# Kernel optimization log

Measured on AMD Instinct MI355X. Metric: run time of the kernel, lower is better.

Reference implementation:

```python
import jax, jax.numpy as jnp
import numpy as np

N_NODES = 50000
N_EDGES = 800000
IN_C, HID_C, OUT_C = 128, 96, 64
BN_EPS = 1e-5


def setup_inputs() -> dict:
    key = jax.random.key(0)
    ks = jax.random.split(key, 12)
    x = jax.random.normal(ks[0], (N_NODES, IN_C), dtype=jnp.float32)
    edge_weight = jax.random.uniform(ks[1], (N_EDGES,), dtype=jnp.float32)
    row = jax.random.randint(ks[2], (N_EDGES,), 0, N_NODES, dtype=jnp.int32)
    col = jax.random.randint(ks[3], (N_EDGES,), 0, N_NODES, dtype=jnp.int32)
    s = 0.05
    W1 = jax.random.normal(ks[4], (IN_C, HID_C), dtype=jnp.float32) * s
    b1 = jnp.zeros((HID_C,), dtype=jnp.float32)
    W2 = jax.random.normal(ks[5], (HID_C, HID_C), dtype=jnp.float32) * s
    b2 = jnp.zeros((HID_C,), dtype=jnp.float32)
    W3 = jax.random.normal(ks[6], (HID_C, OUT_C), dtype=jnp.float32) * s
    b3 = jnp.zeros((OUT_C,), dtype=jnp.float32)
    g1 = jnp.ones((HID_C,), dtype=jnp.float32)
    be1 = jnp.zeros((HID_C,), dtype=jnp.float32)
    g2 = jnp.ones((HID_C,), dtype=jnp.float32)
    be2 = jnp.zeros((HID_C,), dtype=jnp.float32)
    return {"x": x, "edge_weight": edge_weight, "row": row, "col": col,
            "W1": W1, "b1": b1, "W2": W2, "b2": b2, "W3": W3, "b3": b3,
            "g1": g1, "be1": be1, "g2": g2, "be2": be2}


def _gcn_conv(h, edge_weight, row, col, W, b):
    # GCNConv: adj_norm @ (h @ W) + b, adj in COO with normalized edge_weight
    h = h @ W  # [N, d_out]
    msg = edge_weight[:, None] * h[col]  # gather + scale: [E, d_out]
    agg = jax.ops.segment_sum(msg, row, num_segments=N_NODES)  # scatter-add
    return agg + b


def _batch_norm(h, gamma, beta):
    # BatchNorm1d (training-mode batch statistics, biased variance)
    mean = jnp.mean(h, axis=0)
    var = jnp.var(h, axis=0)
    return (h - mean) * jax.lax.rsqrt(var + BN_EPS) * gamma + beta


def reference(x, edge_weight, row, col, W1, b1, W2, b2, W3, b3, g1, be1, g2, be2):
    h = _gcn_conv(x, edge_weight, row, col, W1, b1)
    h = jax.nn.relu(_batch_norm(h, g1, be1))  # dropout is identity in eval
    h = _gcn_conv(h, edge_weight, row, col, W2, b2)
    h = jax.nn.relu(_batch_norm(h, g2, be2))
    h = _gcn_conv(h, edge_weight, row, col, W3, b3)
    return jax.nn.log_softmax(h, axis=-1)
```

## Files before the change

kernel.cpp:

```cpp
#include <hip/hip_runtime.h>
#include <hip/hip_bf16.h>
#include <math.h>

#define N_NODES 50000
#define N_EDGES 800000
#define IN_C 128
#define HID_C 96
#define OUT_C 64
#define BN_EPS 1e-5f

#define ELL_SHIFT 6
#define ELL_CAP   64

#define NGRP 8
#define GRP_ROWS ((N_NODES + NGRP - 1) / NGRP)

#define EW_SCALE 65535.0f
#define EW_INV   (1.0f / 65535.0f)

#define ST_SLICES 4

typedef __attribute__((ext_vector_type(8))) short short8;
typedef __attribute__((ext_vector_type(4))) float f32x4;

static __device__ __forceinline__ unsigned short f2b(float f) {
    __hip_bfloat16 b = __float2bfloat16(f);
    return *reinterpret_cast<unsigned short*>(&b);
}
static __device__ __forceinline__ float b2f(unsigned short u) {
    return __uint_as_float((unsigned)u << 16);
}
static __device__ __forceinline__ unsigned pack2(float a, float b) {
    return (unsigned)f2b(a) | ((unsigned)f2b(b) << 16);
}

#define FMA8(B, V, W)                                          \
    acc[(B) + 0] += (W) * __uint_as_float((V).x << 16);        \
    acc[(B) + 1] += (W) * __uint_as_float((V).x & 0xffff0000u);\
    acc[(B) + 2] += (W) * __uint_as_float((V).y << 16);        \
    acc[(B) + 3] += (W) * __uint_as_float((V).y & 0xffff0000u);\
    acc[(B) + 4] += (W) * __uint_as_float((V).z << 16);        \
    acc[(B) + 5] += (W) * __uint_as_float((V).z & 0xffff0000u);\
    acc[(B) + 6] += (W) * __uint_as_float((V).w << 16);        \
    acc[(B) + 7] += (W) * __uint_as_float((V).w & 0xffff0000u);

__global__ void prep_all(const float* __restrict__ W1, const float* __restrict__ W2,
                         const float* __restrict__ W3,
                         unsigned short* __restrict__ Wt1,
                         unsigned short* __restrict__ Wt2,
                         unsigned short* __restrict__ Wt3,
                         int* __restrict__ cnt, float* __restrict__ stats) {
    int i = blockIdx.x * blockDim.x + threadIdx.x;
    const int n1 = IN_C * HID_C, n2 = HID_C * HID_C, n3 = HID_C * OUT_C;
    if (i < n1) {
        int j = i / IN_C, k = i % IN_C;
        Wt1[i] = f2b(W1[k * HID_C + j]);
    } else if (i < n1 + n2) {
        int t = i - n1, j = t / HID_C, k = t % HID_C;
        Wt2[t] = f2b(W2[k * HID_C + j]);
    } else if (i < n1 + n2 + n3) {
        int t = i - n1 - n2, j = t / HID_C, k = t % HID_C;
        Wt3[t] = f2b(W3[k * OUT_C + j]);
    }
    if (i < N_NODES) cnt[i] = 0;
    if (i < 2 * ST_SLICES * 2 * HID_C) stats[i] = 0.f;
}

__global__ __launch_bounds__(256)
void fill_ell(const int* __restrict__ row, const int* __restrict__ col,
              const float* __restrict__ ew, int* __restrict__ cnt,
              unsigned int* __restrict__ pairs) {
    int g = blockIdx.x & (NGRP - 1);
    int e = (blockIdx.x >> 3) * 256 + threadIdx.x;
    if (e >= N_EDGES) return;
    int r = row[e];
    int lo = g * GRP_ROWS;
    if ((unsigned)(r - lo) >= (unsigned)GRP_ROWS) return;
    int slot = atomicAdd(&cnt[r], 1);
    if (slot < ELL_CAP) {
        unsigned wq = (unsigned)(ew[e] * EW_SCALE + 0.5f);
        pairs[((size_t)r << ELL_SHIFT) + slot] =
            (wq << 16) | (unsigned)col[e];
    }
}

template <int K, int J, bool APPLY, bool XBF16>
__global__ __launch_bounds__(256)
void gemm_mfma(const void* __restrict__ xin,
               const unsigned short* __restrict__ Wt,
               const float* __restrict__ stats,
               const float* __restrict__ gamma,
               const float* __restrict__ beta,
               unsigned short* __restrict__ h, int N) {
    constexpr int MT = 64;
    constexpr int SK = K + 8;
    constexpr int NT = J / 16;
    __shared__ unsigned short Xs[MT * SK];
    __shared__ unsigned short Ws[J * SK];
    __shared__ float scsh_s[APPLY ? 2 * K : 2];

    int tid = threadIdx.x;
    int tileBase = blockIdx.x * MT;

    if (APPLY) {
        if (tid < K) {
            float s = 0.f, sq = 0.f;
#pragma unroll
            for (int sl = 0; sl < ST_SLICES; ++sl) {
                s  += stats[sl * 2 * K + tid];
                sq += stats[sl * 2 * K + K + tid];
            }
            const float invN = 1.f / N_NODES;
            float mean = s * invN;
            float var = sq * invN - mean * mean;
            float sc = gamma[tid] * rsqrtf(var + BN_EPS);
            scsh_s[tid] = sc;
            scsh_s[K + tid] = beta[tid] - mean * sc;
        }
        __syncthreads();
    }

    if (XBF16) {
        const unsigned short* xb = (const unsigned short*)xin;
        for (int i = tid; i < MT * (K / 8); i += 256) {
            int node = i / (K / 8), kq = i % (K / 8);
            int gn = min(tileBase + node, N - 1);
            const unsigned short* src = xb + (size_t)gn * K + kq * 8;
            ushort4 u0 = *(const ushort4*)(src);
            ushort4 u1 = *(const ushort4*)(src + 4);
            if (APPLY) {
                int kb = kq * 8;
                float v0 = fmaxf(b2f(u0.x) * scsh_s[kb + 0] + scsh_s[K + kb + 0], 0.f);
                float v1 = fmaxf(b2f(u0.y) * scsh_s[kb + 1] + scsh_s[K + kb + 1], 0.f);
                float v2 = fmaxf(b2f(u0.z) * scsh_s[kb + 2] + scsh_s[K + kb + 2], 0.f);
                float v3 = fmaxf(b2f(u0.w) * scsh_s[kb + 3] + scsh_s[K + kb + 3], 0.f);
                float v4 = fmaxf(b2f(u1.x) * scsh_s[kb + 4] + scsh_s[K + kb + 4], 0.f);
                float v5 = fmaxf(b2f(u1.y) * scsh_s[kb + 5] + scsh_s[K + kb + 5], 0.f);
                float v6 = fmaxf(b2f(u1.z) * scsh_s[kb + 6] + scsh_s[K + kb + 6], 0.f);
                float v7 = fmaxf(b2f(u1.w) * scsh_s[kb + 7] + scsh_s[K + kb + 7], 0.f);
                u0 = make_ushort4(f2b(v0), f2b(v1), f2b(v2), f2b(v3));
                u1 = make_ushort4(f2b(v4), f2b(v5), f2b(v6), f2b(v7));
            }
            *(ushort4*)&Xs[node * SK + kq * 8] = u0;
            *(ushort4*)&Xs[node * SK + kq * 8 + 4] = u1;
        }
    } else {
        const float* xf = (const float*)xin;
        for (int i = tid; i < MT * (K / 4); i += 256) {
            int node = i / (K / 4), kq = i % (K / 4);
            int gn = min(tileBase + node, N - 1);
            float4 v = *(const float4*)(xf + (size_t)gn * K + kq * 4);
            ushort4 o = make_ushort4(f2b(v.x), f2b(v.y), f2b(v.z), f2b(v.w));
            *(ushort4*)&Xs[node * SK + kq * 4] = o;
        }
    }
    for (int i = tid; i < J * (K / 4); i += 256) {
        int j = i / (K / 4), kq = i % (K / 4);
        *(ushort4*)&Ws[j * SK + kq * 4] =
            *(const ushort4*)(Wt + (size_t)j * K + kq * 4);
    }
    __syncthreads();

    int lane = tid & 63;
    int w = tid >> 6;
    int m16 = lane & 15;
    int quad = lane >> 4;

    f32x4 acc[NT];
#pragma unroll
    for (int nt = 0; nt < NT; ++nt) acc[nt] = (f32x4){0.f, 0.f, 0.f, 0.f};

    const unsigned short* xrow = &Xs[(w * 16 + m16) * SK];
#pragma unroll
    for (int k0 = 0; k0 < K; k0 += 32) {
        short8 a = *(const short8*)(xrow + k0 + quad * 8);
#pragma unroll
        for (int nt = 0; nt < NT; ++nt) {
            short8 b = *(const short8*)&Ws[(nt * 16 + m16) * SK + k0 + quad * 8];
            acc[nt] = __builtin_amdgcn_mfma_f32_16x16x32_bf16(a, b, acc[nt], 0, 0, 0);
        }
    }

#pragma unroll
    for (int nt = 0; nt < NT; ++nt) {
#pragma unroll
        for (int r = 0; r < 4; ++r) {
            int node = tileBase + w * 16 + quad * 4 + r;
            if (node < N)
                h[(size_t)node * J + nt * 16 + m16] = f2b(acc[nt][r]);
        }
    }
}

template <int D, bool LSM, bool STATS>
__global__ __launch_bounds__(256)
void agg_fused(const unsigned short* __restrict__ h,
               const int* __restrict__ cnt,
               const unsigned int* __restrict__ pairs,
               unsigned short* __restrict__ outb,
               float* __restrict__ outf,
               const float* __restrict__ b3,
               float* __restrict__ stats) {
    constexpr int TPN = 4;
    constexpr int C = D / TPN;
    constexpr int NPB = 256 / TPN;
    __shared__ float shS[STATS ? 16 * C : 1];
    __shared__ float shQ[STATS ? 16 * C : 1];

    int tid = threadIdx.x;
    int q = tid & 3;
    int nloc = tid >> 2;
    int n = blockIdx.x * NPB + nloc;
    bool valid = n < N_NODES;
    int nn = valid ? n : N_NODES - 1;
    int end = valid ? min(cnt[nn], ELL_CAP) : 0;
    const unsigned* ep = pairs + ((size_t)nn << ELL_SHIFT);
    const int cbase = q * C;

    float acc[C];
#pragma unroll
    for (int c = 0; c < C; ++c) acc[c] = 0.f;

    int i = 0;
    for (; i + 1 < end; i += 2) {
        unsigned p0 = ep[i], p1 = ep[i + 1];
        float w0 = (float)(p0 >> 16) * EW_INV;
        float w1 = (float)(p1 >> 16) * EW_INV;
        const unsigned short* r0 = h + (size_t)(p0 & 0xFFFFu) * D + cbase;
        const unsigned short* r1 = h + (size_t)(p1 & 0xFFFFu) * D + cbase;
        uint4 v0[C / 8], v1[C / 8];
#pragma unroll
        for (int ch = 0; ch < C / 8; ++ch) v0[ch] = *(const uint4*)(r0 + ch * 8);
#pragma unroll
        for (int ch = 0; ch < C / 8; ++ch) v1[ch] = *(const uint4*)(r1 + ch * 8);
#pragma unroll
        for (int ch = 0; ch < C / 8; ++ch) { FMA8(ch * 8, v0[ch], w0) }
#pragma unroll
        for (int ch = 0; ch < C / 8; ++ch) { FMA8(ch * 8, v1[ch], w1) }
    }
    if (i < end) {
        unsigned p0 = ep[i];
        float w0 = (float)(p0 >> 16) * EW_INV;
        const unsigned short* r0 = h + (size_t)(p0 & 0xFFFFu) * D + cbase;
#pragma unroll
        for (int ch = 0; ch < C / 8; ++ch) {
            uint4 v = *(const uint4*)(r0 + ch * 8);
            FMA8(ch * 8, v, w0)
        }
    }

    if (LSM) {
        float v[C];
#pragma unroll
        for (int c = 0; c < C; ++c) v[c] = acc[c] + b3[cbase + c];
        float m = v[0];
#pragma unroll
        for (int c = 1; c < C; ++c) m = fmaxf(m, v[c]);
        m = fmaxf(m, __shfl_xor(m, 1));
        m = fmaxf(m, __shfl_xor(m, 2));
        float s = 0.f;
#pragma unroll
        for (int c = 0; c < C; ++c) s += expf(v[c] - m);
        s += __shfl_xor(s, 1);
        s += __shfl_xor(s, 2);
        float l = m + logf(s);
        if (valid) {
#pragma unroll
            for (int ch = 0; ch < C / 4; ++ch) {
                float4 o = make_float4(v[ch * 4 + 0] - l, v[ch * 4 + 1] - l,
                                       v[ch * 4 + 2] - l, v[ch * 4 + 3] - l);
                *(float4*)(outf + (size_t)n * D + cbase + ch * 4) = o;
            }
        }
    } else {
#pragma unroll
        for (int c = 0; c < C; ++c) acc[c] = b2f(f2b(acc[c]));
#pragma unroll
        for (int ch = 0; ch < C / 8; ++ch) {
            uint4 o;
            o.x = pack2(acc[ch * 8 + 0], acc[ch * 8 + 1]);
            o.y = pack2(acc[ch * 8 + 2], acc[ch * 8 + 3]);
            o.z = pack2(acc[ch * 8 + 4], acc[ch * 8 + 5]);
            o.w = pack2(acc[ch * 8 + 6], acc[ch * 8 + 7]);
            if (valid)
                *(uint4*)(outb + (size_t)n * D + cbase + ch * 8) = o;
        }
        if (STATS) {
            int lane = tid & 63;
            int wv = tid >> 6;
#pragma unroll
            for (int c = 0; c < C; ++c) {
                float s = acc[c];
                float sq = s * s;
#pragma unroll
                for (int msk = 4; msk < 64; msk <<= 1) {
                    s  += __shfl_xor(s, msk);
                    sq += __shfl_xor(sq, msk);
                }
                if (lane < 4) {
                    shS[(wv * 4 + lane) * C + c] = s;
                    shQ[(wv * 4 + lane) * C + c] = sq;
                }
            }
            __syncthreads();
            if (tid < D) {
                int qq = tid / C, cl = tid % C;
                float S = 0.f, Q = 0.f;
#pragma unroll
                for (int w2 = 0; w2 < 4; ++w2) {
                    S += shS[(w2 * 4 + qq) * C + cl];
                    Q += shQ[(w2 * 4 + qq) * C + cl];
                }
                int slice = blockIdx.x & (ST_SLICES - 1);
                atomicAdd(&stats[slice * 2 * D + tid], S);
                atomicAdd(&stats[slice * 2 * D + D + tid], Q);
            }
        }
    }
}

extern "C" void kernel_launch(void* const* d_in, const int* in_sizes, int n_in,
                              void* d_out, int out_size, void* d_ws, size_t ws_size,
                              hipStream_t stream) {
    const float* x   = (const float*)d_in[0];
    const float* ew  = (const float*)d_in[1];
    const int*   row = (const int*)d_in[2];
    const int*   col = (const int*)d_in[3];
    const float* W1  = (const float*)d_in[4];
    const float* W2  = (const float*)d_in[6];
    const float* W3  = (const float*)d_in[8];
    const float* b3  = (const float*)d_in[9];
    const float* g1  = (const float*)d_in[10];
    const float* be1 = (const float*)d_in[11];
    const float* g2  = (const float*)d_in[12];
    const float* be2 = (const float*)d_in[13];
    float* out = (float*)d_out;

    unsigned short* B      = (unsigned short*)d_ws;
    unsigned short* A      = B + (size_t)N_NODES * HID_C;
    unsigned short* Wt1    = A + (size_t)N_NODES * HID_C;
    unsigned short* Wt2    = Wt1 + IN_C * HID_C;
    unsigned short* Wt3    = Wt2 + HID_C * HID_C;
    unsigned int*   pairs  = (unsigned int*)(Wt3 + HID_C * OUT_C);
    int*            cnt    = (int*)(pairs + ((size_t)N_NODES << ELL_SHIFT));
    float*          stats1 = (float*)(cnt + N_NODES);
    float*          stats2 = stats1 + ST_SLICES * 2 * HID_C;

    const int T = 256;
    const int gridE  = (N_EDGES + T - 1) / T;
    const int gridG  = (N_NODES + 63) / 64;
    const int gridP  = (N_NODES + T - 1) / T;

    prep_all<<<gridP, T, 0, stream>>>(W1, W2, W3, Wt1, Wt2, Wt3, cnt, stats1);
    fill_ell<<<gridE * NGRP, T, 0, stream>>>(row, col, ew, cnt, pairs);

    gemm_mfma<IN_C, HID_C, false, false><<<gridG, T, 0, stream>>>(
        x, Wt1, nullptr, nullptr, nullptr, A, N_NODES);
    agg_fused<HID_C, false, true><<<gridG, T, 0, stream>>>(
        A, cnt, pairs, B, nullptr, nullptr, stats1);

    gemm_mfma<HID_C, HID_C, true, true><<<gridG, T, 0, stream>>>(
        B, Wt2, stats1, g1, be1, A, N_NODES);
    agg_fused<HID_C, false, true><<<gridG, T, 0, stream>>>(
        A, cnt, pairs, B, nullptr, nullptr, stats2);

    gemm_mfma<HID_C, OUT_C, true, true><<<gridG, T, 0, stream>>>(
        B, Wt3, stats2, g2, be2, A, N_NODES);
    agg_fused<OUT_C, true, false><<<gridG, T, 0, stream>>>(
        A, cnt, pairs, nullptr, out, b3, nullptr);
}
```

Before: 266.2 us.

## Fuse all GCN stages into one cooperative persistent kernel with grid syncs

Replaces the eight separate kernel launches with a single cooperative persistent kernel that loops over tiles and uses grid-wide syncs between phases, and overlaps the ELL fill with the first GEMM. The aim is to remove launch overhead and inter-kernel gaps. The cost is lower parallelism: the grid is capped at 768 blocks with strided tile loops, and the kernel now pays for grid barriers and higher register and LDS use. The old multi-kernel path stays as a fallback if the cooperative launch fails.

```diff
diff --git a/kernel.cpp b/kernel.cpp
--- a/kernel.cpp
+++ b/kernel.cpp
@@ -1,6 +1,9 @@
 #include <hip/hip_runtime.h>
+#include <hip/hip_cooperative_groups.h>
 #include <hip/hip_bf16.h>
 #include <math.h>
+
+namespace cg = cooperative_groups;
 
 #define N_NODES 50000
 #define N_EDGES 800000
@@ -19,6 +22,8 @@
 #define EW_INV   (1.0f / 65535.0f)
 
 #define ST_SLICES 4
+
+#define SMEM_BYTES 43584
 
 typedef __attribute__((ext_vector_type(8))) short short8;
 typedef __attribute__((ext_vector_type(4))) float f32x4;
@@ -44,13 +49,11 @@
     acc[(B) + 6] += (W) * __uint_as_float((V).w << 16);        \
     acc[(B) + 7] += (W) * __uint_as_float((V).w & 0xffff0000u);
 
-__global__ void prep_all(const float* __restrict__ W1, const float* __restrict__ W2,
-                         const float* __restrict__ W3,
-                         unsigned short* __restrict__ Wt1,
-                         unsigned short* __restrict__ Wt2,
-                         unsigned short* __restrict__ Wt3,
-                         int* __restrict__ cnt, float* __restrict__ stats) {
-    int i = blockIdx.x * blockDim.x + threadIdx.x;
+
+static __device__ __forceinline__ void prep_body(
+    int i, const float* W1, const float* W2, const float* W3,
+    unsigned short* Wt1, unsigned short* Wt2, unsigned short* Wt3,
+    int* cnt, float* stats) {
     const int n1 = IN_C * HID_C, n2 = HID_C * HID_C, n3 = HID_C * OUT_C;
     if (i < n1) {
         int j = i / IN_C, k = i % IN_C;
@@ -66,22 +69,327 @@
     if (i < 2 * ST_SLICES * 2 * HID_C) stats[i] = 0.f;
 }
 
+static __device__ __forceinline__ void fill_body(
+    int grp, int e, const int* row, const int* col, const float* ew,
+    int* cnt, unsigned int* pairs) {
+    if (e >= N_EDGES) return;
+    int r = row[e];
+    int lo = grp * GRP_ROWS;
+    if ((unsigned)(r - lo) >= (unsigned)GRP_ROWS) return;
+    int slot = atomicAdd(&cnt[r], 1);
+    if (slot < ELL_CAP) {
+        unsigned wq = (unsigned)(ew[e] * EW_SCALE + 0.5f);
+        pairs[((size_t)r << ELL_SHIFT) + slot] = (wq << 16) | (unsigned)col[e];
+    }
+}
+
+template <int K, int J, bool APPLY, bool XBF16>
+static __device__ __forceinline__ void gemm_phase(
+    unsigned char* smem, const void* xin, const unsigned short* Wt,
+    const float* stats, const float* gamma, const float* beta,
+    unsigned short* h, int gridSz) {
+    constexpr int MT = 64;
+    constexpr int SK = K + 8;
+    constexpr int NT = J / 16;
+    unsigned short* Xs = (unsigned short*)smem;
+    unsigned short* Ws = Xs + MT * SK;
+    float* scsh = (float*)(smem + (size_t)(MT + J) * SK * 2);
+
+    int tid = threadIdx.x;
+
+    if (APPLY) {
+        if (tid < K) {
+            float s = 0.f, sq = 0.f;
+#pragma unroll
+            for (int sl = 0; sl < ST_SLICES; ++sl) {
+                s  += stats[sl * 2 * K + tid];
+                sq += stats[sl * 2 * K + K + tid];
+            }
+            const float invN = 1.f / N_NODES;
+            float mean = s * invN;
+            float var = sq * invN - mean * mean;
+            float sc = gamma[tid] * rsqrtf(var + BN_EPS);
+            scsh[tid] = sc;
+            scsh[K + tid] = beta[tid] - mean * sc;
+        }
+    }
+    for (int i = tid; i < J * (K / 4); i += 256) {
+        int j = i / (K / 4), kq = i % (K / 4);
+        *(ushort4*)&Ws[j * SK + kq * 4] =
+            *(const ushort4*)(Wt + (size_t)j * K + kq * 4);
+    }
+    __syncthreads();
+
+    int lane = tid & 63;
+    int w = tid >> 6;
+    int m16 = lane & 15;
+    int quad = lane >> 4;
+    const int nTiles = (N_NODES + MT - 1) / MT;
+
+    for (int tile = blockIdx.x; tile < nTiles; tile += gridSz) {
+        int tileBase = tile * MT;
+
+        if (XBF16) {
+            const unsigned short* xb = (const unsigned short*)xin;
+            for (int i = tid; i < MT * (K / 8); i += 256) {
+                int node = i / (K / 8), kq = i % (K / 8);
+                int gn = min(tileBase + node, N_NODES - 1);
+                const unsigned short* src = xb + (size_t)gn * K + kq * 8;
+                ushort4 u0 = *(const ushort4*)(src);
+                ushort4 u1 = *(const ushort4*)(src + 4);
+                if (APPLY) {
+                    int kb = kq * 8;
+                    float v0 = fmaxf(b2f(u0.x) * scsh[kb + 0] + scsh[K + kb + 0], 0.f);
+                    float v1 = fmaxf(b2f(u0.y) * scsh[kb + 1] + scsh[K + kb + 1], 0.f);
+                    float v2 = fmaxf(b2f(u0.z) * scsh[kb + 2] + scsh[K + kb + 2], 0.f);
+                    float v3 = fmaxf(b2f(u0.w) * scsh[kb + 3] + scsh[K + kb + 3], 0.f);
+                    float v4 = fmaxf(b2f(u1.x) * scsh[kb + 4] + scsh[K + kb + 4], 0.f);
+                    float v5 = fmaxf(b2f(u1.y) * scsh[kb + 5] + scsh[K + kb + 5], 0.f);
+                    float v6 = fmaxf(b2f(u1.z) * scsh[kb + 6] + scsh[K + kb + 6], 0.f);
+                    float v7 = fmaxf(b2f(u1.w) * scsh[kb + 7] + scsh[K + kb + 7], 0.f);
+                    u0 = make_ushort4(f2b(v0), f2b(v1), f2b(v2), f2b(v3));
+                    u1 = make_ushort4(f2b(v4), f2b(v5), f2b(v6), f2b(v7));
+                }
+                *(ushort4*)&Xs[node * SK + kq * 8] = u0;
+                *(ushort4*)&Xs[node * SK + kq * 8 + 4] = u1;
+            }
+        } else {
+            const float* xf = (const float*)xin;
+            for (int i = tid; i < MT * (K / 4); i += 256) {
+                int node = i / (K / 4), kq = i % (K / 4);
+                int gn = min(tileBase + node, N_NODES - 1);
+                float4 v = *(const float4*)(xf + (size_t)gn * K + kq * 4);
+                ushort4 o = make_ushort4(f2b(v.x), f2b(v.y), f2b(v.z), f2b(v.w));
+                *(ushort4*)&Xs[node * SK + kq * 4] = o;
+            }
+        }
+        __syncthreads();
+
+        f32x4 acc[NT];
+#pragma unroll
+        for (int nt = 0; nt < NT; ++nt) acc[nt] = (f32x4){0.f, 0.f, 0.f, 0.f};
+
+        const unsigned short* xrow = &Xs[(w * 16 + m16) * SK];
+#pragma unroll
+        for (int k0 = 0; k0 < K; k0 += 32) {
+            short8 a = *(const short8*)(xrow + k0 + quad * 8);
+#pragma unroll
+            for (int nt = 0; nt < NT; ++nt) {
+                short8 b = *(const short8*)&Ws[(nt * 16 + m16) * SK + k0 + quad * 8];
+                acc[nt] = __builtin_amdgcn_mfma_f32_16x16x32_bf16(a, b, acc[nt], 0, 0, 0);
+            }
+        }
+
+#pragma unroll
+        for (int nt = 0; nt < NT; ++nt) {
+#pragma unroll
+            for (int r = 0; r < 4; ++r) {
+                int node = tileBase + w * 16 + quad * 4 + r;
+                if (node < N_NODES)
+                    h[(size_t)node * J + nt * 16 + m16] = f2b(acc[nt][r]);
+            }
+        }
+        __syncthreads();
+    }
+}
+
+template <int D, bool LSM, bool STATS>
+static __device__ __forceinline__ void agg_phase(
+    unsigned char* smem, const unsigned short* h, const int* cnt,
+    const unsigned int* pairs, unsigned short* outb, float* outf,
+    const float* b3, float* stats, int gridSz) {
+    constexpr int TPN = 4;
+    constexpr int C = D / TPN;
+    constexpr int NPB = 256 / TPN;
+    float* shS = (float*)smem;
+    float* shQ = shS + 16 * C;
+
+    int tid = threadIdx.x;
+    int q = tid & 3;
+    int nloc = tid >> 2;
+    const int nTiles = (N_NODES + NPB - 1) / NPB;
+
+    for (int tile = blockIdx.x; tile < nTiles; tile += gridSz) {
+        int n = tile * NPB + nloc;
+        bool valid = n < N_NODES;
+        int nn = valid ? n : N_NODES - 1;
+        int end = valid ? min(cnt[nn], ELL_CAP) : 0;
+        const unsigned* ep = pairs + ((size_t)nn << ELL_SHIFT);
+        const int cbase = q * C;
+
+        float acc[C];
+#pragma unroll
+        for (int c = 0; c < C; ++c) acc[c] = 0.f;
+
+        int i = 0;
+        for (; i + 1 < end; i += 2) {
+            unsigned p0 = ep[i], p1 = ep[i + 1];
+            float w0 = (float)(p0 >> 16) * EW_INV;
+            float w1 = (float)(p1 >> 16) * EW_INV;
+            const unsigned short* r0 = h + (size_t)(p0 & 0xFFFFu) * D + cbase;
+            const unsigned short* r1 = h + (size_t)(p1 & 0xFFFFu) * D + cbase;
+            uint4 v0[C / 8], v1[C / 8];
+#pragma unroll
+            for (int ch = 0; ch < C / 8; ++ch) v0[ch] = *(const uint4*)(r0 + ch * 8);
+#pragma unroll
+            for (int ch = 0; ch < C / 8; ++ch) v1[ch] = *(const uint4*)(r1 + ch * 8);
+#pragma unroll
+            for (int ch = 0; ch < C / 8; ++ch) { FMA8(ch * 8, v0[ch], w0) }
+#pragma unroll
+            for (int ch = 0; ch < C / 8; ++ch) { FMA8(ch * 8, v1[ch], w1) }
+        }
+        if (i < end) {
+            unsigned p0 = ep[i];
+            float w0 = (float)(p0 >> 16) * EW_INV;
+            const unsigned short* r0 = h + (size_t)(p0 & 0xFFFFu) * D + cbase;
+#pragma unroll
+            for (int ch = 0; ch < C / 8; ++ch) {
+                uint4 v = *(const uint4*)(r0 + ch * 8);
+                FMA8(ch * 8, v, w0)
+            }
+        }
+
+        if (LSM) {
+            float v[C];
+#pragma unroll
+            for (int c = 0; c < C; ++c) v[c] = acc[c] + b3[cbase + c];
+            float m = v[0];
+#pragma unroll
+            for (int c = 1; c < C; ++c) m = fmaxf(m, v[c]);
+            m = fmaxf(m, __shfl_xor(m, 1));
+            m = fmaxf(m, __shfl_xor(m, 2));
+            float s = 0.f;
+#pragma unroll
+            for (int c = 0; c < C; ++c) s += expf(v[c] - m);
+            s += __shfl_xor(s, 1);
+            s += __shfl_xor(s, 2);
+            float l = m + logf(s);
+            if (valid) {
+#pragma unroll
+                for (int ch = 0; ch < C / 4; ++ch) {
+                    float4 o = make_float4(v[ch * 4 + 0] - l, v[ch * 4 + 1] - l,
+                                           v[ch * 4 + 2] - l, v[ch * 4 + 3] - l);
+                    *(float4*)(outf + (size_t)n * D + cbase + ch * 4) = o;
+                }
+            }
+        } else {
+#pragma unroll
+            for (int c = 0; c < C; ++c) acc[c] = b2f(f2b(acc[c]));
+#pragma unroll
+            for (int ch = 0; ch < C / 8; ++ch) {
+                uint4 o;
+                o.x = pack2(acc[ch * 8 + 0], acc[ch * 8 + 1]);
+                o.y = pack2(acc[ch * 8 + 2], acc[ch * 8 + 3]);
+                o.z = pack2(acc[ch * 8 + 4], acc[ch * 8 + 5]);
+                o.w = pack2(acc[ch * 8 + 6], acc[ch * 8 + 7]);
+                if (valid)
+                    *(uint4*)(outb + (size_t)n * D + cbase + ch * 8) = o;
+            }
+            if (STATS) {
+                int lane = tid & 63;
+                int wv = tid >> 6;
+#pragma unroll
+                for (int c = 0; c < C; ++c) {
+                    float s = acc[c];
+                    float sq = s * s;
+#pragma unroll
+                    for (int msk = 4; msk < 64; msk <<= 1) {
+                        s  += __shfl_xor(s, msk);
+                        sq += __shfl_xor(sq, msk);
+                    }
+                    if (lane < 4) {
+                        shS[(wv * 4 + lane) * C + c] = s;
+                        shQ[(wv * 4 + lane) * C + c] = sq;
+                    }
+                }
+                __syncthreads();
+                if (tid < D) {
+                    int qq = tid / C, cl = tid % C;
+                    float S = 0.f, Q = 0.f;
+#pragma unroll
+                    for (int w2 = 0; w2 < 4; ++w2) {
+                        S += shS[(w2 * 4 + qq) * C + cl];
+                        Q += shQ[(w2 * 4 + qq) * C + cl];
+                    }
+                    int slice = blockIdx.x & (ST_SLICES - 1);
+                    atomicAdd(&stats[slice * 2 * D + tid], S);
+                    atomicAdd(&stats[slice * 2 * D + D + tid], Q);
+                }
+                __syncthreads();
+            }
+        }
+    }
+}
+
+struct MegaParams {
+    const float *x, *ew;
+    const int *row, *col;
+    const float *W1, *W2, *W3, *b3, *g1, *be1, *g2, *be2;
+    unsigned short *B, *A, *Wt1, *Wt2, *Wt3;
+    unsigned int *pairs;
+    int *cnt;
+    float *stats1, *stats2, *out;
+};
+
+__global__ __launch_bounds__(256)
+void mega(MegaParams p) {
+    __shared__ __align__(16) unsigned char smem[SMEM_BYTES];
+    cg::grid_group grid = cg::this_grid();
+    const int G = (int)gridDim.x;
+
+    for (int i = blockIdx.x * 256 + threadIdx.x; i < N_NODES; i += G * 256)
+        prep_body(i, p.W1, p.W2, p.W3, p.Wt1, p.Wt2, p.Wt3, p.cnt, p.stats1);
+    grid.sync();
+
+    gemm_phase<IN_C, HID_C, false, false>(smem, p.x, p.Wt1,
+                                          nullptr, nullptr, nullptr, p.A, G);
+    {
+        const int nUnits = (N_EDGES + 255) / 256;
+        int grp = blockIdx.x & (NGRP - 1);
+        for (int u = blockIdx.x >> 3; u < nUnits; u += (G >> 3))
+            fill_body(grp, u * 256 + threadIdx.x, p.row, p.col, p.ew,
+                      p.cnt, p.pairs);
+    }
+    grid.sync();
+
+    agg_phase<HID_C, false, true>(smem, p.A, p.cnt, p.pairs, p.B,
+                                  nullptr, nullptr, p.stats1, G);
+    grid.sync();
+
+    gemm_phase<HID_C, HID_C, true, true>(smem, p.B, p.Wt2,
+                                         p.stats1, p.g1, p.be1, p.A, G);
+    grid.sync();
+
+    agg_phase<HID_C, false, true>(smem, p.A, p.cnt, p.pairs, p.B,
+                                  nullptr, nullptr, p.stats2, G);
+    grid.sync();
+
+    gemm_phase<HID_C, OUT_C, true, true>(smem, p.B, p.Wt3,
+                                         p.stats2, p.g2, p.be2, p.A, G);
+    grid.sync();
+
+    agg_phase<OUT_C, true, false>(smem, p.A, p.cnt, p.pairs, nullptr,
+                                  p.out, p.b3, nullptr, G);
+}
+
+__global__ void prep_all(const float* __restrict__ W1, const float* __restrict__ W2,
+                         const float* __restrict__ W3,
+                         unsigned short* __restrict__ Wt1,
+                         unsigned short* __restrict__ Wt2,
+                         unsigned short* __restrict__ Wt3,
+                         int* __restrict__ cnt, float* __restrict__ stats) {
+    int i = blockIdx.x * blockDim.x + threadIdx.x;
+    if (i < N_NODES)
+        prep_body(i, W1, W2, W3, Wt1, Wt2, Wt3, cnt, stats);
+}
+
 __global__ __launch_bounds__(256)
 void fill_ell(const int* __restrict__ row, const int* __restrict__ col,
               const float* __restrict__ ew, int* __restrict__ cnt,
               unsigned int* __restrict__ pairs) {
-    int g = blockIdx.x & (NGRP - 1);
+    int grp = blockIdx.x & (NGRP - 1);
     int e = (blockIdx.x >> 3) * 256 + threadIdx.x;
-    if (e >= N_EDGES) return;
-    int r = row[e];
-    int lo = g * GRP_ROWS;
-    if ((unsigned)(r - lo) >= (unsigned)GRP_ROWS) return;
-    int slot = atomicAdd(&cnt[r], 1);
-    if (slot < ELL_CAP) {
-        unsigned wq = (unsigned)(ew[e] * EW_SCALE + 0.5f);
-        pairs[((size_t)r << ELL_SHIFT) + slot] =
-            (wq << 16) | (unsigned)col[e];
-    }
+    fill_body(grp, e, row, col, ew, cnt, pairs);
 }
 
 template <int K, int J, bool APPLY, bool XBF16>
@@ -91,105 +399,10 @@
                const float* __restrict__ stats,
                const float* __restrict__ gamma,
                const float* __restrict__ beta,
-               unsigned short* __restrict__ h, int N) {
-    constexpr int MT = 64;
-    constexpr int SK = K + 8;
-    constexpr int NT = J / 16;
-    __shared__ unsigned short Xs[MT * SK];
-    __shared__ unsigned short Ws[J * SK];
-    __shared__ float scsh_s[APPLY ? 2 * K : 2];
-
-    int tid = threadIdx.x;
-    int tileBase = blockIdx.x * MT;
-
-    if (APPLY) {
-        if (tid < K) {
-            float s = 0.f, sq = 0.f;
-#pragma unroll
-            for (int sl = 0; sl < ST_SLICES; ++sl) {
-                s  += stats[sl * 2 * K + tid];
-                sq += stats[sl * 2 * K + K + tid];
-            }
-            const float invN = 1.f / N_NODES;
-            float mean = s * invN;
-            float var = sq * invN - mean * mean;
-            float sc = gamma[tid] * rsqrtf(var + BN_EPS);
-            scsh_s[tid] = sc;
-            scsh_s[K + tid] = beta[tid] - mean * sc;
-        }
-        __syncthreads();
-    }
-
-    if (XBF16) {
-        const unsigned short* xb = (const unsigned short*)xin;
-        for (int i = tid; i < MT * (K / 8); i += 256) {
-            int node = i / (K / 8), kq = i % (K / 8);
-            int gn = min(tileBase + node, N - 1);
-            const unsigned short* src = xb + (size_t)gn * K + kq * 8;
-            ushort4 u0 = *(const ushort4*)(src);
-            ushort4 u1 = *(const ushort4*)(src + 4);
-            if (APPLY) {
-                int kb = kq * 8;
-                float v0 = fmaxf(b2f(u0.x) * scsh_s[kb + 0] + scsh_s[K + kb + 0], 0.f);
-                float v1 = fmaxf(b2f(u0.y) * scsh_s[kb + 1] + scsh_s[K + kb + 1], 0.f);
-                float v2 = fmaxf(b2f(u0.z) * scsh_s[kb + 2] + scsh_s[K + kb + 2], 0.f);
-                float v3 = fmaxf(b2f(u0.w) * scsh_s[kb + 3] + scsh_s[K + kb + 3], 0.f);
-                float v4 = fmaxf(b2f(u1.x) * scsh_s[kb + 4] + scsh_s[K + kb + 4], 0.f);
-                float v5 = fmaxf(b2f(u1.y) * scsh_s[kb + 5] + scsh_s[K + kb + 5], 0.f);
-                float v6 = fmaxf(b2f(u1.z) * scsh_s[kb + 6] + scsh_s[K + kb + 6], 0.f);
-                float v7 = fmaxf(b2f(u1.w) * scsh_s[kb + 7] + scsh_s[K + kb + 7], 0.f);
-                u0 = make_ushort4(f2b(v0), f2b(v1), f2b(v2), f2b(v3));
-                u1 = make_ushort4(f2b(v4), f2b(v5), f2b(v6), f2b(v7));
-            }
-            *(ushort4*)&Xs[node * SK + kq * 8] = u0;
-            *(ushort4*)&Xs[node * SK + kq * 8 + 4] = u1;
-        }
-    } else {
-        const float* xf = (const float*)xin;
-        for (int i = tid; i < MT * (K / 4); i += 256) {
-            int node = i / (K / 4), kq = i % (K / 4);
-            int gn = min(tileBase + node, N - 1);
-            float4 v = *(const float4*)(xf + (size_t)gn * K + kq * 4);
-            ushort4 o = make_ushort4(f2b(v.x), f2b(v.y), f2b(v.z), f2b(v.w));
-            *(ushort4*)&Xs[node * SK + kq * 4] = o;
-        }
-    }
-    for (int i = tid; i < J * (K / 4); i += 256) {
-        int j = i / (K / 4), kq = i % (K / 4);
-        *(ushort4*)&Ws[j * SK + kq * 4] =
-            *(const ushort4*)(Wt + (size_t)j * K + kq * 4);
-    }
-    __syncthreads();
-
-    int lane = tid & 63;
-    int w = tid >> 6;
-    int m16 = lane & 15;
-    int quad = lane >> 4;
-
-    f32x4 acc[NT];
-#pragma unroll
-    for (int nt = 0; nt < NT; ++nt) acc[nt] = (f32x4){0.f, 0.f, 0.f, 0.f};
-
-    const unsigned short* xrow = &Xs[(w * 16 + m16) * SK];
-#pragma unroll
-    for (int k0 = 0; k0 < K; k0 += 32) {
-        short8 a = *(const short8*)(xrow + k0 + quad * 8);
-#pragma unroll
-        for (int nt = 0; nt < NT; ++nt) {
-            short8 b = *(const short8*)&Ws[(nt * 16 + m16) * SK + k0 + quad * 8];
-            acc[nt] = __builtin_amdgcn_mfma_f32_16x16x32_bf16(a, b, acc[nt], 0, 0, 0);
-        }
-    }
-
-#pragma unroll
-    for (int nt = 0; nt < NT; ++nt) {
-#pragma unroll
-        for (int r = 0; r < 4; ++r) {
-            int node = tileBase + w * 16 + quad * 4 + r;
-            if (node < N)
-                h[(size_t)node * J + nt * 16 + m16] = f2b(acc[nt][r]);
-        }
-    }
+               unsigned short* __restrict__ h) {
+    __shared__ __align__(16) unsigned char smem[SMEM_BYTES];
+    gemm_phase<K, J, APPLY, XBF16>(smem, xin, Wt, stats, gamma, beta, h,
+                                   (int)gridDim.x);
 }
 
 template <int D, bool LSM, bool STATS>
@@ -201,122 +414,9 @@
                float* __restrict__ outf,
                const float* __restrict__ b3,
                float* __restrict__ stats) {
-    constexpr int TPN = 4;
-    constexpr int C = D / TPN;
-    constexpr int NPB = 256 / TPN;
-    __shared__ float shS[STATS ? 16 * C : 1];
-    __shared__ float shQ[STATS ? 16 * C : 1];
-
-    int tid = threadIdx.x;
-    int q = tid & 3;
-    int nloc = tid >> 2;
-    int n = blockIdx.x * NPB + nloc;
-    bool valid = n < N_NODES;
-    int nn = valid ? n : N_NODES - 1;
-    int end = valid ? min(cnt[nn], ELL_CAP) : 0;
-    const unsigned* ep = pairs + ((size_t)nn << ELL_SHIFT);
-    const int cbase = q * C;
-
-    float acc[C];
-#pragma unroll
-    for (int c = 0; c < C; ++c) acc[c] = 0.f;
-
-    int i = 0;
-    for (; i + 1 < end; i += 2) {
-        unsigned p0 = ep[i], p1 = ep[i + 1];
-        float w0 = (float)(p0 >> 16) * EW_INV;
-        float w1 = (float)(p1 >> 16) * EW_INV;
-        const unsigned short* r0 = h + (size_t)(p0 & 0xFFFFu) * D + cbase;
-        const unsigned short* r1 = h + (size_t)(p1 & 0xFFFFu) * D + cbase;
-        uint4 v0[C / 8], v1[C / 8];
-#pragma unroll
-        for (int ch = 0; ch < C / 8; ++ch) v0[ch] = *(const uint4*)(r0 + ch * 8);
-#pragma unroll
-        for (int ch = 0; ch < C / 8; ++ch) v1[ch] = *(const uint4*)(r1 + ch * 8);
-#pragma unroll
-        for (int ch = 0; ch < C / 8; ++ch) { FMA8(ch * 8, v0[ch], w0) }
-#pragma unroll
-        for (int ch = 0; ch < C / 8; ++ch) { FMA8(ch * 8, v1[ch], w1) }
-    }
-    if (i < end) {
-        unsigned p0 = ep[i];
-        float w0 = (float)(p0 >> 16) * EW_INV;
-        const unsigned short* r0 = h + (size_t)(p0 & 0xFFFFu) * D + cbase;
-#pragma unroll
-        for (int ch = 0; ch < C / 8; ++ch) {
-            uint4 v = *(const uint4*)(r0 + ch * 8);
-            FMA8(ch * 8, v, w0)
-        }
-    }
-
-    if (LSM) {
-        float v[C];
-#pragma unroll
-        for (int c = 0; c < C; ++c) v[c] = acc[c] + b3[cbase + c];
-        float m = v[0];
-#pragma unroll
-        for (int c = 1; c < C; ++c) m = fmaxf(m, v[c]);
-        m = fmaxf(m, __shfl_xor(m, 1));
-        m = fmaxf(m, __shfl_xor(m, 2));
-        float s = 0.f;
-#pragma unroll
-        for (int c = 0; c < C; ++c) s += expf(v[c] - m);
-        s += __shfl_xor(s, 1);
-        s += __shfl_xor(s, 2);
-        float l = m + logf(s);
-        if (valid) {
-#pragma unroll
-            for (int ch = 0; ch < C / 4; ++ch) {
-                float4 o = make_float4(v[ch * 4 + 0] - l, v[ch * 4 + 1] - l,
-                                       v[ch * 4 + 2] - l, v[ch * 4 + 3] - l);
-                *(float4*)(outf + (size_t)n * D + cbase + ch * 4) = o;
-            }
-        }
-    } else {
-#pragma unroll
-        for (int c = 0; c < C; ++c) acc[c] = b2f(f2b(acc[c]));
-#pragma unroll
-        for (int ch = 0; ch < C / 8; ++ch) {
-            uint4 o;
-            o.x = pack2(acc[ch * 8 + 0], acc[ch * 8 + 1]);
-            o.y = pack2(acc[ch * 8 + 2], acc[ch * 8 + 3]);
-            o.z = pack2(acc[ch * 8 + 4], acc[ch * 8 + 5]);
-            o.w = pack2(acc[ch * 8 + 6], acc[ch * 8 + 7]);
-            if (valid)
-                *(uint4*)(outb + (size_t)n * D + cbase + ch * 8) = o;
-        }
-        if (STATS) {
-            int lane = tid & 63;
-            int wv = tid >> 6;
-#pragma unroll
-            for (int c = 0; c < C; ++c) {
-                float s = acc[c];
-                float sq = s * s;
-#pragma unroll
-                for (int msk = 4; msk < 64; msk <<= 1) {
-                    s  += __shfl_xor(s, msk);
-                    sq += __shfl_xor(sq, msk);
-                }
-                if (lane < 4) {
-                    shS[(wv * 4 + lane) * C + c] = s;
-                    shQ[(wv * 4 + lane) * C + c] = sq;
-                }
-            }
-            __syncthreads();
-            if (tid < D) {
-                int qq = tid / C, cl = tid % C;
-                float S = 0.f, Q = 0.f;
-#pragma unroll
-                for (int w2 = 0; w2 < 4; ++w2) {
-                    S += shS[(w2 * 4 + qq) * C + cl];
-                    Q += shQ[(w2 * 4 + qq) * C + cl];
-                }
-                int slice = blockIdx.x & (ST_SLICES - 1);
-                atomicAdd(&stats[slice * 2 * D + tid], S);
-                atomicAdd(&stats[slice * 2 * D + D + tid], Q);
-            }
-        }
-    }
+    __shared__ __align__(16) unsigned char smem[4096];
+    agg_phase<D, LSM, STATS>(smem, h, cnt, pairs, outb, outf, b3, stats,
+                             (int)gridDim.x);
 }
 
 extern "C" void kernel_launch(void* const* d_in, const int* in_sizes, int n_in,
@@ -346,26 +446,51 @@
     float*          stats1 = (float*)(cnt + N_NODES);
     float*          stats2 = stats1 + ST_SLICES * 2 * HID_C;
 
-    const int T = 256;
-    const int gridE  = (N_EDGES + T - 1) / T;
-    const int gridG  = (N_NODES + 63) / 64;
-    const int gridP  = (N_NODES + T - 1) / T;
-
-    prep_all<<<gridP, T, 0, stream>>>(W1, W2, W3, Wt1, Wt2, Wt3, cnt, stats1);
-    fill_ell<<<gridE * NGRP, T, 0, stream>>>(row, col, ew, cnt, pairs);
-
-    gemm_mfma<IN_C, HID_C, false, false><<<gridG, T, 0, stream>>>(
-        x, Wt1, nullptr, nullptr, nullptr, A, N_NODES);
-    agg_fused<HID_C, false, true><<<gridG, T, 0, stream>>>(
-        A, cnt, pairs, B, nullptr, nullptr, stats1);
-
-    gemm_mfma<HID_C, HID_C, true, true><<<gridG, T, 0, stream>>>(
-        B, Wt2, stats1, g1, be1, A, N_NODES);
-    agg_fused<HID_C, false, true><<<gridG, T, 0, stream>>>(
-        A, cnt, pairs, B, nullptr, nullptr, stats2);
-
-    gemm_mfma<HID_C, OUT_C, true, true><<<gridG, T, 0, stream>>>(
-        B, Wt3, stats2, g2, be2, A, N_NODES);
-    agg_fused<OUT_C, true, false><<<gridG, T, 0, stream>>>(
-        A, cnt, pairs, nullptr, out, b3, nullptr);
-}
+    MegaParams P;
+    P.x = x; P.ew = ew; P.row = row; P.col = col;
+    P.W1 = W1; P.W2 = W2; P.W3 = W3; P.b3 = b3;
+    P.g1 = g1; P.be1 = be1; P.g2 = g2; P.be2 = be2;
+    P.B = B; P.A = A; P.Wt1 = Wt1; P.Wt2 = Wt2; P.Wt3 = Wt3;
+    P.pairs = pairs; P.cnt = cnt; P.stats1 = stats1; P.stats2 = stats2;
+    P.out = out;
+
+    bool done = false;
+    int nb = 0;
+    if (hipOccupancyMaxActiveBlocksPerMultiprocessor(&nb, mega, 256, 0)
+            == hipSuccess && nb > 0) {
+        int G = nb * 256;
+        if (G > 768) G = 768;
+        G &= ~15;
+        if (G >= 16) {
+            void* args[] = { (void*)&P };
+            if (hipLaunchCooperativeKernel(mega, dim3(G), dim3(256),
+                                           args, 0, stream) == hipSuccess)
+                done = true;
+        }
+    }
+
+    if (!done) {
+        const int T = 256;
+        const int gridE = (N_EDGES + T - 1) / T;
+        const int gridG = (N_NODES + 63) / 64;
+        const int gridP = (N_NODES + T - 1) / T;
+
+        prep_all<<<gridP, T, 0, stream>>>(W1, W2, W3, Wt1, Wt2, Wt3, cnt, stats1);
+        fill_ell<<<gridE * NGRP, T, 0, stream>>>(row, col, ew, cnt, pairs);
+
+        gemm_mfma<IN_C, HID_C, false, false><<<gridG, T, 0, stream>>>(
+            x, Wt1, nullptr, nullptr, nullptr, A);
+        agg_fused<HID_C, false, true><<<gridG, T, 0, stream>>>(
+            A, cnt, pairs, B, nullptr, nullptr, stats1);
+
+        gemm_mfma<HID_C, HID_C, true, true><<<gridG, T, 0, stream>>>(
+            B, Wt2, stats1, g1, be1, A);
+        agg_fused<HID_C, false, true><<<gridG, T, 0, stream>>>(
+            A, cnt, pairs, B, nullptr, nullptr, stats2);
+
+        gemm_mfma<HID_C, OUT_C, true, true><<<gridG, T, 0, stream>>>(
+            B, Wt3, stats2, g2, be2, A);
+        agg_fused<OUT_C, true, false><<<gridG, T, 0, stream>>>(
+            A, cnt, pairs, nullptr, out, b3, nullptr);
+    }
+}
```

After: 602.0 us. 126% more time.

## Store hidden features in 24-channel column slices and aggregate per slice

Applied to the files above, without the earlier changes.

Hidden activations are now written by the GEMM in a sliced layout: four planes of 24 bf16 channels per node. A new agg_sliced kernel assigns one thread per node per slice, so each gathered neighbor row is a compact 48-byte chunk. The intent is to shrink each gather's working set so it fits in cache. Edge-pair loads become nontemporal, and the final layer gets a dedicated log-softmax aggregation kernel. Trade-offs: the edge list is read four times, accesses within a wave are less coalesced, and the interleaved slice-to-block mapping may keep all slices resident at once.

```diff
diff --git a/kernel.cpp b/kernel.cpp
--- a/kernel.cpp
+++ b/kernel.cpp
@@ -19,6 +19,8 @@
 #define EW_INV   (1.0f / 65535.0f)
 
 #define ST_SLICES 4
+
+#define SLC 24
 
 typedef __attribute__((ext_vector_type(8))) short short8;
 typedef __attribute__((ext_vector_type(4))) float f32x4;
@@ -79,12 +81,11 @@
     int slot = atomicAdd(&cnt[r], 1);
     if (slot < ELL_CAP) {
         unsigned wq = (unsigned)(ew[e] * EW_SCALE + 0.5f);
-        pairs[((size_t)r << ELL_SHIFT) + slot] =
-            (wq << 16) | (unsigned)col[e];
-    }
-}
-
-template <int K, int J, bool APPLY, bool XBF16>
+        pairs[((size_t)r << ELL_SHIFT) + slot] = (wq << 16) | (unsigned)col[e];
+    }
+}
+
+template <int K, int J, bool APPLY, bool XBF16, bool SLICED>
 __global__ __launch_bounds__(256)
 void gemm_mfma(const void* __restrict__ xin,
                const unsigned short* __restrict__ Wt,
@@ -125,7 +126,8 @@
         for (int i = tid; i < MT * (K / 8); i += 256) {
             int node = i / (K / 8), kq = i % (K / 8);
             int gn = min(tileBase + node, N - 1);
-            const unsigned short* src = xb + (size_t)gn * K + kq * 8;
+            const unsigned short* src =
+                xb + ((size_t)(kq / 3) * N_NODES + gn) * SLC + (kq % 3) * 8;
             ushort4 u0 = *(const ushort4*)(src);
             ushort4 u1 = *(const ushort4*)(src + 4);
             if (APPLY) {
@@ -186,31 +188,116 @@
 #pragma unroll
         for (int r = 0; r < 4; ++r) {
             int node = tileBase + w * 16 + quad * 4 + r;
-            if (node < N)
-                h[(size_t)node * J + nt * 16 + m16] = f2b(acc[nt][r]);
-        }
-    }
-}
-
-template <int D, bool LSM, bool STATS>
+            if (node < N) {
+                int c = nt * 16 + m16;
+                if (SLICED) {
+                    int q = c / SLC, off = c - q * SLC;
+                    h[((size_t)q * N_NODES + node) * SLC + off] = f2b(acc[nt][r]);
+                } else {
+                    h[(size_t)node * J + c] = f2b(acc[nt][r]);
+                }
+            }
+        }
+    }
+}
+
 __global__ __launch_bounds__(256)
-void agg_fused(const unsigned short* __restrict__ h,
-               const int* __restrict__ cnt,
-               const unsigned int* __restrict__ pairs,
-               unsigned short* __restrict__ outb,
-               float* __restrict__ outf,
-               const float* __restrict__ b3,
-               float* __restrict__ stats) {
-    constexpr int TPN = 4;
-    constexpr int C = D / TPN;
-    constexpr int NPB = 256 / TPN;
-    __shared__ float shS[STATS ? 16 * C : 1];
-    __shared__ float shQ[STATS ? 16 * C : 1];
-
+void agg_sliced(const unsigned short* __restrict__ A,
+                const int* __restrict__ cnt,
+                const unsigned int* __restrict__ pairs,
+                unsigned short* __restrict__ B,
+                float* __restrict__ stats) {
+    constexpr int C = SLC;
+    int tid = threadIdx.x;
+    int q = blockIdx.x & 3;
+    int gb = blockIdx.x >> 2;
+    int n = gb * 256 + tid;
+    bool valid = n < N_NODES;
+    int nn = valid ? n : N_NODES - 1;
+    int end = valid ? min(cnt[nn], ELL_CAP) : 0;
+    const unsigned* ep = pairs + ((size_t)nn << ELL_SHIFT);
+    const unsigned short* hq = A + (size_t)q * N_NODES * C;
+
+    float acc[C];
+#pragma unroll
+    for (int c = 0; c < C; ++c) acc[c] = 0.f;
+
+    int i = 0;
+    for (; i + 1 < end; i += 2) {
+        unsigned p0 = __builtin_nontemporal_load(ep + i);
+        unsigned p1 = __builtin_nontemporal_load(ep + i + 1);
+        float w0 = (float)(p0 >> 16) * EW_INV;
+        float w1 = (float)(p1 >> 16) * EW_INV;
+        const uint4* r0 = (const uint4*)(hq + (size_t)(p0 & 0xFFFFu) * C);
+        const uint4* r1 = (const uint4*)(hq + (size_t)(p1 & 0xFFFFu) * C);
+        uint4 v00 = r0[0], v01 = r0[1], v02 = r0[2];
+        uint4 v10 = r1[0], v11 = r1[1], v12 = r1[2];
+        FMA8(0, v00, w0) FMA8(8, v01, w0) FMA8(16, v02, w0)
+        FMA8(0, v10, w1) FMA8(8, v11, w1) FMA8(16, v12, w1)
+    }
+    if (i < end) {
+        unsigned p0 = __builtin_nontemporal_load(ep + i);
+        float w0 = (float)(p0 >> 16) * EW_INV;
+        const uint4* r0 = (const uint4*)(hq + (size_t)(p0 & 0xFFFFu) * C);
+        uint4 v00 = r0[0], v01 = r0[1], v02 = r0[2];
+        FMA8(0, v00, w0) FMA8(8, v01, w0) FMA8(16, v02, w0)
+    }
+
+#pragma unroll
+    for (int c = 0; c < C; ++c) acc[c] = b2f(f2b(acc[c]));
+
+    if (valid) {
+        uint4 o0, o1, o2;
+        o0.x = pack2(acc[0], acc[1]);   o0.y = pack2(acc[2], acc[3]);
+        o0.z = pack2(acc[4], acc[5]);   o0.w = pack2(acc[6], acc[7]);
+        o1.x = pack2(acc[8], acc[9]);   o1.y = pack2(acc[10], acc[11]);
+        o1.z = pack2(acc[12], acc[13]); o1.w = pack2(acc[14], acc[15]);
+        o2.x = pack2(acc[16], acc[17]); o2.y = pack2(acc[18], acc[19]);
+        o2.z = pack2(acc[20], acc[21]); o2.w = pack2(acc[22], acc[23]);
+        uint4* dst = (uint4*)(B + ((size_t)q * N_NODES + n) * C);
+        dst[0] = o0; dst[1] = o1; dst[2] = o2;
+    }
+
+    __shared__ float shS[4 * C];
+    __shared__ float shQ[4 * C];
+    int lane = tid & 63, wv = tid >> 6;
+#pragma unroll
+    for (int c = 0; c < C; ++c) {
+        float s = acc[c];
+        float sq = s * s;
+#pragma unroll
+        for (int msk = 1; msk < 64; msk <<= 1) {
+            s  += __shfl_xor(s, msk);
+            sq += __shfl_xor(sq, msk);
+        }
+        if (lane == 0) { shS[wv * C + c] = s; shQ[wv * C + c] = sq; }
+    }
+    __syncthreads();
+    if (tid < C) {
+        float S = 0.f, Q = 0.f;
+#pragma unroll
+        for (int w2 = 0; w2 < 4; ++w2) {
+            S += shS[w2 * C + tid];
+            Q += shQ[w2 * C + tid];
+        }
+        int sl = gb & (ST_SLICES - 1);
+        atomicAdd(&stats[sl * 2 * HID_C + q * C + tid], S);
+        atomicAdd(&stats[sl * 2 * HID_C + HID_C + q * C + tid], Q);
+    }
+}
+
+__global__ __launch_bounds__(256)
+void agg_lsm(const unsigned short* __restrict__ h,
+             const int* __restrict__ cnt,
+             const unsigned int* __restrict__ pairs,
+             float* __restrict__ outf,
+             const float* __restrict__ b3) {
+    constexpr int D = OUT_C;
+    constexpr int C = D / 4;
     int tid = threadIdx.x;
     int q = tid & 3;
     int nloc = tid >> 2;
-    int n = blockIdx.x * NPB + nloc;
+    int n = blockIdx.x * 64 + nloc;
     bool valid = n < N_NODES;
     int nn = valid ? n : N_NODES - 1;
     int end = valid ? min(cnt[nn], ELL_CAP) : 0;
@@ -223,98 +310,45 @@
 
     int i = 0;
     for (; i + 1 < end; i += 2) {
-        unsigned p0 = ep[i], p1 = ep[i + 1];
+        unsigned p0 = __builtin_nontemporal_load(ep + i);
+        unsigned p1 = __builtin_nontemporal_load(ep + i + 1);
         float w0 = (float)(p0 >> 16) * EW_INV;
         float w1 = (float)(p1 >> 16) * EW_INV;
-        const unsigned short* r0 = h + (size_t)(p0 & 0xFFFFu) * D + cbase;
-        const unsigned short* r1 = h + (size_t)(p1 & 0xFFFFu) * D + cbase;
-        uint4 v0[C / 8], v1[C / 8];
-#pragma unroll
-        for (int ch = 0; ch < C / 8; ++ch) v0[ch] = *(const uint4*)(r0 + ch * 8);
-#pragma unroll
-        for (int ch = 0; ch < C / 8; ++ch) v1[ch] = *(const uint4*)(r1 + ch * 8);
-#pragma unroll
-        for (int ch = 0; ch < C / 8; ++ch) { FMA8(ch * 8, v0[ch], w0) }
-#pragma unroll
-        for (int ch = 0; ch < C / 8; ++ch) { FMA8(ch * 8, v1[ch], w1) }
+        const uint4* r0 = (const uint4*)(h + (size_t)(p0 & 0xFFFFu) * D + cbase);
+        const uint4* r1 = (const uint4*)(h + (size_t)(p1 & 0xFFFFu) * D + cbase);
+        uint4 v00 = r0[0], v01 = r0[1];
+        uint4 v10 = r1[0], v11 = r1[1];
+        FMA8(0, v00, w0) FMA8(8, v01, w0)
+        FMA8(0, v10, w1) FMA8(8, v11, w1)
     }
     if (i < end) {
-        unsigned p0 = ep[i];
+        unsigned p0 = __builtin_nontemporal_load(ep + i);
         float w0 = (float)(p0 >> 16) * EW_INV;
-        const unsigned short* r0 = h + (size_t)(p0 & 0xFFFFu) * D + cbase;
-#pragma unroll
-        for (int ch = 0; ch < C / 8; ++ch) {
-            uint4 v = *(const uint4*)(r0 + ch * 8);
-            FMA8(ch * 8, v, w0)
-        }
-    }
-
-    if (LSM) {
-        float v[C];
-#pragma unroll
-        for (int c = 0; c < C; ++c) v[c] = acc[c] + b3[cbase + c];
-        float m = v[0];
-#pragma unroll
-        for (int c = 1; c < C; ++c) m = fmaxf(m, v[c]);
-        m = fmaxf(m, __shfl_xor(m, 1));
-        m = fmaxf(m, __shfl_xor(m, 2));
-        float s = 0.f;
-#pragma unroll
-        for (int c = 0; c < C; ++c) s += expf(v[c] - m);
-        s += __shfl_xor(s, 1);
-        s += __shfl_xor(s, 2);
-        float l = m + logf(s);
-        if (valid) {
-#pragma unroll
-            for (int ch = 0; ch < C / 4; ++ch) {
-                float4 o = make_float4(v[ch * 4 + 0] - l, v[ch * 4 + 1] - l,
-                                       v[ch * 4 + 2] - l, v[ch * 4 + 3] - l);
-                *(float4*)(outf + (size_t)n * D + cbase + ch * 4) = o;
-            }
-        }
-    } else {
-#pragma unroll
-        for (int c = 0; c < C; ++c) acc[c] = b2f(f2b(acc[c]));
-#pragma unroll
-        for (int ch = 0; ch < C / 8; ++ch) {
-            uint4 o;
-            o.x = pack2(acc[ch * 8 + 0], acc[ch * 8 + 1]);
-            o.y = pack2(acc[ch * 8 + 2], acc[ch * 8 + 3]);
-            o.z = pack2(acc[ch * 8 + 4], acc[ch * 8 + 5]);
-            o.w = pack2(acc[ch * 8 + 6], acc[ch * 8 + 7]);
-            if (valid)
-                *(uint4*)(outb + (size_t)n * D + cbase + ch * 8) = o;
-        }
-        if (STATS) {
-            int lane = tid & 63;
-            int wv = tid >> 6;
-#pragma unroll
-            for (int c = 0; c < C; ++c) {
-                float s = acc[c];
-                float sq = s * s;
-#pragma unroll
-                for (int msk = 4; msk < 64; msk <<= 1) {
-                    s  += __shfl_xor(s, msk);
-                    sq += __shfl_xor(sq, msk);
-                }
-                if (lane < 4) {
-                    shS[(wv * 4 + lane) * C + c] = s;
-                    shQ[(wv * 4 + lane) * C + c] = sq;
-                }
-            }
-            __syncthreads();
-            if (tid < D) {
-                int qq = tid / C, cl = tid % C;
-                float S = 0.f, Q = 0.f;
-#pragma unroll
-                for (int w2 = 0; w2 < 4; ++w2) {
-                    S += shS[(w2 * 4 + qq) * C + cl];
-                    Q += shQ[(w2 * 4 + qq) * C + cl];
-                }
-                int slice = blockIdx.x & (ST_SLICES - 1);
-                atomicAdd(&stats[slice * 2 * D + tid], S);
-                atomicAdd(&stats[slice * 2 * D + D + tid], Q);
-            }
+        const uint4* r0 = (const uint4*)(h + (size_t)(p0 & 0xFFFFu) * D + cbase);
+        uint4 v00 = r0[0], v01 = r0[1];
+        FMA8(0, v00, w0) FMA8(8, v01, w0)
+    }
+
+    float v[C];
+#pragma unroll
+    for (int c = 0; c < C; ++c) v[c] = acc[c] + b3[cbase + c];
+    float m = v[0];
+#pragma unroll
+    for (int c = 1; c < C; ++c) m = fmaxf(m, v[c]);
+    m = fmaxf(m, __shfl_xor(m, 1));
+    m = fmaxf(m, __shfl_xor(m, 2));
+    float s = 0.f;
+#pragma unroll
+    for (int c = 0; c < C; ++c) s += expf(v[c] - m);
+    s += __shfl_xor(s, 1);
+    s += __shfl_xor(s, 2);
+    float l = m + logf(s);
+    if (valid) {
+#pragma unroll
+        for (int ch = 0; ch < C / 4; ++ch) {
+            float4 o = make_float4(v[ch * 4 + 0] - l, v[ch * 4 + 1] - l,
+                                   v[ch * 4 + 2] - l, v[ch * 4 + 3] - l);
+            *(float4*)(outf + (size_t)n * D + cbase + ch * 4) = o;
         }
     }
 }
@@ -349,23 +383,21 @@
     const int T = 256;
     const int gridE  = (N_EDGES + T - 1) / T;
     const int gridG  = (N_NODES + 63) / 64;
+    const int gridS  = 4 * ((N_NODES + 255) / 256);
     const int gridP  = (N_NODES + T - 1) / T;
 
     prep_all<<<gridP, T, 0, stream>>>(W1, W2, W3, Wt1, Wt2, Wt3, cnt, stats1);
     fill_ell<<<gridE * NGRP, T, 0, stream>>>(row, col, ew, cnt, pairs);
 
-    gemm_mfma<IN_C, HID_C, false, false><<<gridG, T, 0, stream>>>(
+    gemm_mfma<IN_C, HID_C, false, false, true><<<gridG, T, 0, stream>>>(
         x, Wt1, nullptr, nullptr, nullptr, A, N_NODES);
-    agg_fused<HID_C, false, true><<<gridG, T, 0, stream>>>(
-        A, cnt, pairs, B, nullptr, nullptr, stats1);
-
-    gemm_mfma<HID_C, HID_C, true, true><<<gridG, T, 0, stream>>>(
+    agg_sliced<<<gridS, T, 0, stream>>>(A, cnt, pairs, B, stats1);
+
+    gemm_mfma<HID_C, HID_C, true, true, true><<<gridG, T, 0, stream>>>(
         B, Wt2, stats1, g1, be1, A, N_NODES);
-    agg_fused<HID_C, false, true><<<gridG, T, 0, stream>>>(
-        A, cnt, pairs, B, nullptr, nullptr, stats2);
-
-    gemm_mfma<HID_C, OUT_C, true, true><<<gridG, T, 0, stream>>>(
+    agg_sliced<<<gridS, T, 0, stream>>>(A, cnt, pairs, B, stats2);
+
+    gemm_mfma<HID_C, OUT_C, true, true, false><<<gridG, T, 0, stream>>>(
         B, Wt3, stats2, g2, be2, A, N_NODES);
-    agg_fused<OUT_C, true, false><<<gridG, T, 0, stream>>>(
-        A, cnt, pairs, nullptr, out, b3, nullptr);
-}
+    agg_lsm<<<gridG, T, 0, stream>>>(A, cnt, pairs, out, b3);
+}
```

After: 339.0 us. +27.4%, slower.
